# Performance work log

Hardware: AMD Instinct MI355X
Metric: run time of the kernel (lower is better)

## Reference

```python
import jax, jax.numpy as jnp
import numpy as np

N_NODES = 50000


def gcn_layer(x, W, b, src, dst, norm):
    # x: [N, Fin] -> [N, Fout]; PyG GCNConv: x' = D^-1/2 (A+I) D^-1/2 (x W) + b
    h = x @ W
    msg = h[src] * norm[:, None]              # gather + scale per edge (incl. self loops)
    out = jax.ops.segment_sum(msg, dst, num_segments=N_NODES)
    return out + b


def setup_inputs() -> dict:
    key = jax.random.key(0)
    ks = jax.random.split(key, 12)
    F_in, F_hid, T, E = 128, 128, 10, 1600000
    features = jax.random.normal(ks[0], (N_NODES, F_in), dtype=jnp.float32)
    edges = jax.random.randint(ks[1], (2, E), 0, N_NODES, dtype=jnp.int64)
    s = 1.0 / np.sqrt(F_in)
    W0 = jax.random.uniform(ks[2], (F_in, F_hid), jnp.float32, -s, s)
    b0 = jnp.zeros((F_hid,), jnp.float32)
    W1 = jax.random.uniform(ks[3], (F_hid, F_hid), jnp.float32, -s, s)
    b1 = jnp.zeros((F_hid,), jnp.float32)
    W2 = jax.random.uniform(ks[4], (F_hid, F_hid), jnp.float32, -s, s)
    b2 = jnp.zeros((F_hid,), jnp.float32)
    Wout = jax.random.uniform(ks[5], (F_hid, T), jnp.float32, -s, s)
    bout = jax.random.uniform(ks[6], (T,), jnp.float32, -s, s)
    return {"features": features, "edges": edges, "W0": W0, "b0": b0,
            "W1": W1, "b1": b1, "W2": W2, "b2": b2, "Wout": Wout, "bout": bout}


def reference(features, edges, W0, b0, W1, b1, W2, b2, Wout, bout):
    # Add self loops once; edge structure shared across layers.
    loop = jnp.arange(N_NODES, dtype=edges.dtype)
    src = jnp.concatenate([edges[0], loop])
    dst = jnp.concatenate([edges[1], loop])
    deg = jax.ops.segment_sum(jnp.ones_like(dst, dtype=features.dtype), dst,
                              num_segments=N_NODES)
    dinv = jnp.where(deg > 0, jax.lax.rsqrt(deg), 0.0)
    norm = dinv[src] * dinv[dst]              # [E + N]

    x = gcn_layer(features, W0, b0, src, dst, norm)
    x = gcn_layer(x, W1, b1, src, dst, norm)
    x = gcn_layer(x, W2, b2, src, dst, norm)

    pooled = jnp.mean(x, axis=0)              # [F_hid]
    logits = pooled @ Wout + bout             # [T]
    return jax.nn.log_softmax(logits, axis=0).reshape(1, -1)
```

## Files before the change

### kernel.cpp

```cpp
#include <hip/hip_runtime.h>


#define FDIM 128
#define HSZ 12500
#define NBG 64
#define NB_V0 512
#define S_FIX 16777216.0f
#define INV_S (1.0f / 16777216.0f)


__global__ void __launch_bounds__(1024)
hist_deg_kernel(const int* __restrict__ edges, int E, int e4, int N,
                int* __restrict__ partial) {
  __shared__ int h[HSZ];
  const int g = blockIdx.x / NBG;
  const int j = blockIdx.x - g * NBG;
  const int lo = g * HSZ;
  const int hi = min(N, lo + HSZ);
  const int hs = hi - lo;
  for (int i = threadIdx.x; i < hs; i += blockDim.x) h[i] = 0;
  __syncthreads();
  const int* dst = edges + E;
  const int4* dst4 = (const int4*)dst;
  for (int i = j * blockDim.x + threadIdx.x; i < e4; i += NBG * blockDim.x) {
    int4 d = dst4[i];
    if (d.x >= lo && d.x < hi) atomicAdd(&h[d.x - lo], 1);
    if (d.y >= lo && d.y < hi) atomicAdd(&h[d.y - lo], 1);
    if (d.z >= lo && d.z < hi) atomicAdd(&h[d.z - lo], 1);
    if (d.w >= lo && d.w < hi) atomicAdd(&h[d.w - lo], 1);
  }
  if (j == 0) {
    for (int e = 4 * e4 + threadIdx.x; e < E; e += blockDim.x) {
      int d = dst[e];
      if (d >= lo && d < hi) atomicAdd(&h[d - lo], 1);
    }
  }
  __syncthreads();
  int* out = partial + (size_t)blockIdx.x * HSZ;
  for (int i = threadIdx.x; i < hs; i += blockDim.x) out[i] = h[i];
}

__global__ void merge_dinv_kernel(const int* __restrict__ partial,
                                  float* __restrict__ dinv, int N) {
  int n = blockIdx.x * blockDim.x + threadIdx.x;
  if (n >= N) return;
  int g = n / HSZ;
  int off = n - g * HSZ;
  const int* p = partial + ((size_t)g * NBG) * HSZ + off;
  int s = 1;
  for (int jj = 0; jj < NBG; ++jj) s += p[(size_t)jj * HSZ];
  dinv[n] = rsqrtf((float)s);
}

__global__ void __launch_bounds__(1024)
hist_u_kernel(const int* __restrict__ edges, int E, int e4, int N,
              const float* __restrict__ w,
              float* __restrict__ partial) {
  __shared__ float h[HSZ];
  const int g = blockIdx.x / NBG;
  const int j = blockIdx.x - g * NBG;
  const int lo = g * HSZ;
  const int hi = min(N, lo + HSZ);
  const int hs = hi - lo;
  for (int i = threadIdx.x; i < hs; i += blockDim.x) h[i] = 0.f;
  __syncthreads();
  const int4* s4 = (const int4*)edges;
  const int4* d4 = (const int4*)(edges + E);
  for (int i = j * blockDim.x + threadIdx.x; i < e4; i += NBG * blockDim.x) {
    int4 s = s4[i];
    int4 d = d4[i];
    if (s.x >= lo && s.x < hi) atomicAdd(&h[s.x - lo], w[d.x]);
    if (s.y >= lo && s.y < hi) atomicAdd(&h[s.y - lo], w[d.y]);
    if (s.z >= lo && s.z < hi) atomicAdd(&h[s.z - lo], w[d.z]);
    if (s.w >= lo && s.w < hi) atomicAdd(&h[s.w - lo], w[d.w]);
  }
  if (j == 0) {
    const int* se = edges; const int* de = edges + E;
    for (int e = 4 * e4 + threadIdx.x; e < E; e += blockDim.x) {
      int s = se[e], d = de[e];
      if (s >= lo && s < hi) atomicAdd(&h[s - lo], w[d]);
    }
  }
  __syncthreads();
  float* out = partial + (size_t)blockIdx.x * HSZ;
  for (int i = threadIdx.x; i < hs; i += blockDim.x) out[i] = h[i];
}

__global__ void __launch_bounds__(256)
merge_u_kernel(const float* __restrict__ partial,
               const float* __restrict__ dinv,
               const float* __restrict__ win,
               float* __restrict__ uout,
               float* __restrict__ wout,
               float* __restrict__ ssump, int N) {
  __shared__ float red[4];
  int n = blockIdx.x * blockDim.x + threadIdx.x;
  float u = 0.f;
  if (n < N) {
    int g = n / HSZ;
    int off = n - g * HSZ;
    const float* p = partial + ((size_t)g * NBG) * HSZ + off;
    float s = 0.f;
    for (int jj = 0; jj < NBG; ++jj) s += p[(size_t)jj * HSZ];
    u = dinv[n] * (s + win[n]);
    if (uout) uout[n] = u;
    if (wout) wout[n] = dinv[n] * u;
  }
  if (ssump) {
    float a = u;
    for (int o = 32; o > 0; o >>= 1) a += __shfl_down(a, o, 64);
    if ((threadIdx.x & 63) == 0) red[threadIdx.x >> 6] = a;
    __syncthreads();
    if (threadIdx.x == 0)
      ssump[blockIdx.x] = red[0] + red[1] + red[2] + red[3];
  }
}

__global__ void v0_kernel(const float* __restrict__ feat,
                          const float* __restrict__ u0,
                          float* __restrict__ v0p, int N) {
  __shared__ float sh[2][FDIM];
  int f = threadIdx.x & (FDIM - 1);
  int r2 = threadIdx.x >> 7;
  float acc = 0.f;
  for (int r = blockIdx.x * 2 + r2; r < N; r += gridDim.x * 2)
    acc += u0[r] * feat[(size_t)r * FDIM + f];
  sh[r2][f] = acc;
  __syncthreads();
  if (r2 == 0) v0p[(size_t)blockIdx.x * FDIM + f] = sh[0][f] + sh[1][f];
}

__global__ void __launch_bounds__(1024)
final_kernel(const float* __restrict__ W0, const float* __restrict__ b0,
             const float* __restrict__ W1, const float* __restrict__ b1,
             const float* __restrict__ W2, const float* __restrict__ b2,
             const float* __restrict__ Wout, const float* __restrict__ bout,
             const float* __restrict__ v0p, int nv0,
             const float* __restrict__ ssumpA,
             const float* __restrict__ ssumpB,
             int nss,
             float* __restrict__ out, int N) {
  __shared__ float Wl[FDIM * FDIM];
  __shared__ float WoL[FDIM * 10];
  __shared__ float va[FDIM], vb[FDIM];
  __shared__ float part[8][FDIM];
  __shared__ float red0[16], red1[16];
  __shared__ float shS1, shS2;
  __shared__ float lg[10];
  const int t = threadIdx.x;
  const int f = t & (FDIM - 1);
  const int sl = t >> 7;

  {
    const float4* w4 = (const float4*)W0;
    float4* l4 = (float4*)Wl;
    #pragma unroll
    for (int i = 0; i < 4; ++i) l4[t + i * 1024] = w4[t + i * 1024];
    if (t < (FDIM * 10) / 4) ((float4*)WoL)[t] = ((const float4*)Wout)[t];
  }
  float acc = 0.f;
  for (int j = sl; j < nv0; j += 8) acc += v0p[(size_t)j * FDIM + f];
  part[sl][f] = acc;
  {
    float a0 = 0.f, a1 = 0.f;
    for (int j = t; j < nss; j += 1024) { a0 += ssumpA[j]; a1 += ssumpB[j]; }
    for (int o = 32; o > 0; o >>= 1) {
      a0 += __shfl_down(a0, o, 64);
      a1 += __shfl_down(a1, o, 64);
    }
    if ((t & 63) == 0) { red0[t >> 6] = a0; red1[t >> 6] = a1; }
  }
  __syncthreads();
  if (sl == 0) {
    float s = 0.f;
    #pragma unroll
    for (int j = 0; j < 8; ++j) s += part[j][f];
    va[f] = s;
  }
  if (t == 0) {
    float x = 0.f, y = 0.f;
    #pragma unroll
    for (int i = 0; i < 16; ++i) { x += red0[i]; y += red1[i]; }
    shS2 = x; shS1 = y;
  }
  __syncthreads();

  acc = 0.f;
  #pragma unroll
  for (int k = 0; k < 16; ++k) {
    int kk = sl * 16 + k;
    acc += va[kk] * Wl[kk * FDIM + f];
  }
  part[sl][f] = acc;
  __syncthreads();
  {
    const float4* w4 = (const float4*)W1;
    float4* l4 = (float4*)Wl;
    #pragma unroll
    for (int i = 0; i < 4; ++i) l4[t + i * 1024] = w4[t + i * 1024];
  }
  if (sl == 0) {
    float s = 0.f;
    #pragma unroll
    for (int j = 0; j < 8; ++j) s += part[j][f];
    vb[f] = s + shS1 * b0[f];
  }
  __syncthreads();

  acc = 0.f;
  #pragma unroll
  for (int k = 0; k < 16; ++k) {
    int kk = sl * 16 + k;
    acc += vb[kk] * Wl[kk * FDIM + f];
  }
  part[sl][f] = acc;
  __syncthreads();
  {
    const float4* w4 = (const float4*)W2;
    float4* l4 = (float4*)Wl;
    #pragma unroll
    for (int i = 0; i < 4; ++i) l4[t + i * 1024] = w4[t + i * 1024];
  }
  if (sl == 0) {
    float s = 0.f;
    #pragma unroll
    for (int j = 0; j < 8; ++j) s += part[j][f];
    va[f] = s + shS2 * b1[f];
  }
  __syncthreads();

  acc = 0.f;
  #pragma unroll
  for (int k = 0; k < 16; ++k) {
    int kk = sl * 16 + k;
    acc += va[kk] * Wl[kk * FDIM + f];
  }
  part[sl][f] = acc;
  __syncthreads();
  if (sl == 0) {
    float s = 0.f;
    #pragma unroll
    for (int j = 0; j < 8; ++j) s += part[j][f];
    vb[f] = s / (float)N + b2[f];
  }
  __syncthreads();

  if (t < 10) {
    float a = 0.f;
    for (int k = 0; k < FDIM; ++k) a += vb[k] * WoL[k * 10 + t];
    lg[t] = a + bout[t];
  }
  __syncthreads();
  if (t == 0) {
    float m = lg[0];
    for (int q = 1; q < 10; ++q) m = fmaxf(m, lg[q]);
    float s = 0.f;
    for (int q = 0; q < 10; ++q) s += expf(lg[q] - m);
    float lse = logf(s);
    for (int q = 0; q < 10; ++q) out[q] = lg[q] - m - lse;
  }
}


__global__ void deg_kernel(const int* __restrict__ edges, int E, int M,
                           int* __restrict__ deg) {
  for (int e = blockIdx.x * blockDim.x + threadIdx.x; e < M;
       e += gridDim.x * blockDim.x) {
    int d = (e < E) ? edges[E + e] : (e - E);
    atomicAdd(&deg[d], 1);
  }
}

__global__ void dinv_kernel(const int* __restrict__ deg,
                            float* __restrict__ dinv, int N) {
  int i = blockIdx.x * blockDim.x + threadIdx.x;
  if (i < N) {
    float d = (float)deg[i];
    dinv[i] = (d > 0.f) ? rsqrtf(d) : 0.f;
  }
}

__global__ void upass_kernel(const int* __restrict__ edges, int E, int M,
                             const float* __restrict__ dinv,
                             const int* __restrict__ uin_q,
                             int* __restrict__ uout_q) {
  for (int e = blockIdx.x * blockDim.x + threadIdx.x; e < M;
       e += gridDim.x * blockDim.x) {
    int s, d;
    if (e < E) { s = edges[e]; d = edges[E + e]; }
    else       { s = e - E;    d = s; }
    float v = dinv[s] * dinv[d];
    if (uin_q) v *= (float)uin_q[d] * INV_S;
    atomicAdd(&uout_q[s], __float2int_rn(v * S_FIX));
  }
}

__global__ void sums_kernel(const int* __restrict__ u2q,
                            const int* __restrict__ u1q,
                            float* __restrict__ ssump, int N) {
  __shared__ float red[8];
  int i = blockIdx.x * blockDim.x + threadIdx.x;
  float a = 0.f, b = 0.f;
  if (i < N) { a = (float)u2q[i] * INV_S; b = (float)u1q[i] * INV_S; }
  for (int o = 32; o > 0; o >>= 1) {
    a += __shfl_down(a, o, 64);
    b += __shfl_down(b, o, 64);
  }
  if ((threadIdx.x & 63) == 0) {
    red[(threadIdx.x >> 6) * 2] = a;
    red[(threadIdx.x >> 6) * 2 + 1] = b;
  }
  __syncthreads();
  if (threadIdx.x == 0) {
    ssump[blockIdx.x] = red[0] + red[2] + red[4] + red[6];
    ssump[gridDim.x + blockIdx.x] = red[1] + red[3] + red[5] + red[7];
  }
}

__global__ void v0_fallback_kernel(const float* __restrict__ feat,
                                   const int* __restrict__ u0q,
                                   float* __restrict__ v0p, int N) {
  __shared__ float sh[2][FDIM];
  int f = threadIdx.x & (FDIM - 1);
  int r2 = threadIdx.x >> 7;
  float acc = 0.f;
  for (int r = blockIdx.x * 2 + r2; r < N; r += gridDim.x * 2)
    acc += ((float)u0q[r] * INV_S) * feat[(size_t)r * FDIM + f];
  sh[r2][f] = acc;
  __syncthreads();
  if (r2 == 0) v0p[(size_t)blockIdx.x * FDIM + f] = sh[0][f] + sh[1][f];
}


extern "C" void kernel_launch(void* const* d_in, const int* in_sizes, int n_in,
                              void* d_out, int out_size, void* d_ws, size_t ws_size,
                              hipStream_t stream) {
  const float* feat = (const float*)d_in[0];
  const int*   edges = (const int*)d_in[1];
  const float* W0 = (const float*)d_in[2];
  const float* b0 = (const float*)d_in[3];
  const float* W1 = (const float*)d_in[4];
  const float* b1 = (const float*)d_in[5];
  const float* W2 = (const float*)d_in[6];
  const float* b2 = (const float*)d_in[7];
  const float* Wout = (const float*)d_in[8];
  const float* bout = (const float*)d_in[9];

  const int N = in_sizes[0] / FDIM;
  const int E = in_sizes[1] / 2;
  const int NG = (N + HSZ - 1) / HSZ;
  const int e4 = ((E & 3) == 0) ? (E >> 2) : 0;
  const int mergeGrid = (N + 255) / 256;

  char* ws = (char*)d_ws;
  size_t nb = ((size_t)N * 4 + 511) & ~(size_t)511;
  size_t partB = ((size_t)NG * NBG * HSZ * 4 + 511) & ~(size_t)511;
  size_t v0pB = (size_t)NB_V0 * FDIM * 4;
  size_t ssB = ((size_t)mergeGrid * 4 + 511) & ~(size_t)511;
  size_t need = partB + 4 * nb + v0pB + 2 * ssB;

  if (ws_size >= need) {
    char* p = ws;
    void*  part = (void*)p;        p += partB;
    float* dinv = (float*)p;       p += nb;
    float* w2   = (float*)p;       p += nb;
    float* w1   = (float*)p;       p += nb;
    float* u0   = (float*)p;       p += nb;
    float* v0p  = (float*)p;       p += v0pB;
    float* ssA  = (float*)p;       p += ssB;
    float* ssB_ = (float*)p;

    hist_deg_kernel<<<NG * NBG, 1024, 0, stream>>>(edges, E, e4, N, (int*)part);
    merge_dinv_kernel<<<mergeGrid, 256, 0, stream>>>((const int*)part, dinv, N);
    hist_u_kernel<<<NG * NBG, 1024, 0, stream>>>(edges, E, e4, N, dinv, (float*)part);
    merge_u_kernel<<<mergeGrid, 256, 0, stream>>>((const float*)part, dinv, dinv,
                                                  nullptr, w2, ssA, N);
    hist_u_kernel<<<NG * NBG, 1024, 0, stream>>>(edges, E, e4, N, w2, (float*)part);
    merge_u_kernel<<<mergeGrid, 256, 0, stream>>>((const float*)part, dinv, w2,
                                                  nullptr, w1, ssB_, N);
    hist_u_kernel<<<NG * NBG, 1024, 0, stream>>>(edges, E, e4, N, w1, (float*)part);
    merge_u_kernel<<<mergeGrid, 256, 0, stream>>>((const float*)part, dinv, w1,
                                                  u0, nullptr, nullptr, N);
    v0_kernel<<<NB_V0, 256, 0, stream>>>(feat, u0, v0p, N);
    final_kernel<<<1, 1024, 0, stream>>>(W0, b0, W1, b1, W2, b2, Wout, bout,
                                         v0p, NB_V0, ssA, ssB_, mergeGrid,
                                         (float*)d_out, N);
  } else {
    const int M = E + N;
    int*   deg  = (int*)(ws);
    float* dinv = (float*)(ws + nb);
    int*   u2q  = (int*)(ws + 2 * nb);
    int*   u1q  = (int*)(ws + 3 * nb);
    int*   u0q  = (int*)(ws + 4 * nb);
    float* v0p  = (float*)(ws + 5 * nb);
    float* ssp  = (float*)(ws + 5 * nb + v0pB);

    hipMemsetAsync(ws, 0, 5 * nb, stream);

    deg_kernel<<<2048, 256, 0, stream>>>(edges, E, M, deg);
    dinv_kernel<<<mergeGrid, 256, 0, stream>>>(deg, dinv, N);
    upass_kernel<<<2048, 256, 0, stream>>>(edges, E, M, dinv, nullptr, u2q);
    upass_kernel<<<2048, 256, 0, stream>>>(edges, E, M, dinv, u2q, u1q);
    upass_kernel<<<2048, 256, 0, stream>>>(edges, E, M, dinv, u1q, u0q);
    sums_kernel<<<mergeGrid, 256, 0, stream>>>(u2q, u1q, ssp, N);
    v0_fallback_kernel<<<NB_V0, 256, 0, stream>>>(feat, u0q, v0p, N);
    final_kernel<<<1, 1024, 0, stream>>>(W0, b0, W1, b1, W2, b2, Wout, bout,
                                         v0p, NB_V0, ssp, ssp + mergeGrid,
                                         mergeGrid, (float*)d_out, N);
  }
}
```

Before: 125.3 us.

## Bucket edges by source range once so histogram passes read only their slice

Adds count, scan and scatter kernels that sort edges into four buckets by source-node range, each edge packed as a local source index and a destination in one int. The three weighted-histogram passes then read only their group's bucket instead of rescanning all edges with range filters, which cuts their global traffic about eightfold. The v0 reduction is also reshaped to fewer blocks with more threads each. The packing assumes destinations fit in 16 bits (N=50000) and exactly four groups, which is only guarded by NG==4, and the one-time scatter costs three extra launches plus a full pass over the edges.

```diff
diff --git a/kernel.cpp b/kernel.cpp
--- a/kernel.cpp
+++ b/kernel.cpp
@@ -4,9 +4,124 @@
 #define FDIM 128
 #define HSZ 12500
 #define NBG 64
-#define NB_V0 512
+#define NB_V0 128
 #define S_FIX 16777216.0f
 #define INV_S (1.0f / 16777216.0f)
+
+
+__global__ void __launch_bounds__(256)
+count_kernel(const int* __restrict__ edges, int E, int e4,
+             int* __restrict__ blockCnt) {
+  __shared__ int cnt[4];
+  if (threadIdx.x < 4) cnt[threadIdx.x] = 0;
+  __syncthreads();
+  int c0 = 0, c1 = 0, c2 = 0, c3 = 0;
+  const int4* s4 = (const int4*)edges;
+  for (int i = blockIdx.x * 256 + threadIdx.x; i < e4; i += 256 * 256) {
+    int4 s = s4[i];
+    int g;
+    g = s.x / HSZ; if (g == 0) ++c0; else if (g == 1) ++c1; else if (g == 2) ++c2; else ++c3;
+    g = s.y / HSZ; if (g == 0) ++c0; else if (g == 1) ++c1; else if (g == 2) ++c2; else ++c3;
+    g = s.z / HSZ; if (g == 0) ++c0; else if (g == 1) ++c1; else if (g == 2) ++c2; else ++c3;
+    g = s.w / HSZ; if (g == 0) ++c0; else if (g == 1) ++c1; else if (g == 2) ++c2; else ++c3;
+  }
+  if (blockIdx.x == 0) {
+    for (int e = 4 * e4 + threadIdx.x; e < E; e += 256) {
+      int g = edges[e] / HSZ;
+      if (g == 0) ++c0; else if (g == 1) ++c1; else if (g == 2) ++c2; else ++c3;
+    }
+  }
+  for (int o = 32; o > 0; o >>= 1) {
+    c0 += __shfl_down(c0, o, 64);
+    c1 += __shfl_down(c1, o, 64);
+    c2 += __shfl_down(c2, o, 64);
+    c3 += __shfl_down(c3, o, 64);
+  }
+  if ((threadIdx.x & 63) == 0) {
+    atomicAdd(&cnt[0], c0);
+    atomicAdd(&cnt[1], c1);
+    atomicAdd(&cnt[2], c2);
+    atomicAdd(&cnt[3], c3);
+  }
+  __syncthreads();
+  if (threadIdx.x < 4) blockCnt[blockIdx.x * 4 + threadIdx.x] = cnt[threadIdx.x];
+}
+
+__global__ void __launch_bounds__(256)
+scan_kernel(const int* __restrict__ blockCnt, int* __restrict__ blockOff,
+            int* __restrict__ meta) {
+  __shared__ int c[256 * 4];
+  __shared__ int totS[4], baseS[4];
+  for (int i = threadIdx.x; i < 256 * 4; i += 256) c[i] = blockCnt[i];
+  __syncthreads();
+  if (threadIdx.x < 4) {
+    int g = threadIdx.x, run = 0;
+    for (int b = 0; b < 256; ++b) {
+      int v = c[b * 4 + g];
+      c[b * 4 + g] = run;
+      run += v;
+    }
+    totS[g] = run;
+  }
+  __syncthreads();
+  if (threadIdx.x == 0) {
+    int b = 0;
+    for (int g = 0; g < 4; ++g) { baseS[g] = b; b += totS[g]; }
+  }
+  __syncthreads();
+  for (int i = threadIdx.x; i < 256 * 4; i += 256)
+    blockOff[i] = c[i] + baseS[i & 3];
+  if (threadIdx.x < 4) {
+    meta[threadIdx.x] = baseS[threadIdx.x];
+    meta[4 + threadIdx.x] = totS[threadIdx.x];
+  }
+}
+
+__device__ __forceinline__ void push_edge(int s, int d, int lane, int w,
+                                          int* off, volatile int* wbase,
+                                          int* __restrict__ bucket) {
+  int g = s / HSZ;
+  unsigned long long m0 = __ballot(g == 0);
+  unsigned long long m1 = __ballot(g == 1);
+  unsigned long long m2 = __ballot(g == 2);
+  unsigned long long m3 = __ballot(g == 3);
+  unsigned long long mg = (g == 0) ? m0 : (g == 1) ? m1 : (g == 2) ? m2 : m3;
+  #pragma unroll
+  for (int k = 0; k < 4; ++k) {
+    unsigned long long mk = (k == 0) ? m0 : (k == 1) ? m1 : (k == 2) ? m2 : m3;
+    int ck = __popcll(mk);
+    if (ck && lane == __ffsll((unsigned long long)mk) - 1)
+      wbase[w * 4 + k] = atomicAdd(&off[k], ck);
+  }
+  int rank = __popcll(mg & ((1ull << lane) - 1ull));
+  bucket[wbase[w * 4 + g] + rank] = ((s - g * HSZ) << 16) | d;
+}
+
+__global__ void __launch_bounds__(256)
+scatter_kernel(const int* __restrict__ edges, int E, int e4,
+               const int* __restrict__ blockOff, int* __restrict__ bucket) {
+  __shared__ int off[4];
+  __shared__ int wbase[4 * 4];
+  if (threadIdx.x < 4) off[threadIdx.x] = blockOff[blockIdx.x * 4 + threadIdx.x];
+  __syncthreads();
+  const int lane = threadIdx.x & 63;
+  const int w = threadIdx.x >> 6;
+  const int4* s4 = (const int4*)edges;
+  const int4* d4 = (const int4*)(edges + E);
+  for (int i = blockIdx.x * 256 + threadIdx.x; i < e4; i += 256 * 256) {
+    int4 s = s4[i];
+    int4 d = d4[i];
+    push_edge(s.x, d.x, lane, w, off, wbase, bucket);
+    push_edge(s.y, d.y, lane, w, off, wbase, bucket);
+    push_edge(s.z, d.z, lane, w, off, wbase, bucket);
+    push_edge(s.w, d.w, lane, w, off, wbase, bucket);
+  }
+  if (blockIdx.x == 0) {
+    for (int e = 4 * e4 + threadIdx.x; e < E; e += 256) {
+      push_edge(edges[e], edges[E + e], lane, w, off, wbase, bucket);
+    }
+  }
+}
 
 
 __global__ void __launch_bounds__(1024)
@@ -53,37 +168,25 @@
 }
 
 __global__ void __launch_bounds__(1024)
-hist_u_kernel(const int* __restrict__ edges, int E, int e4, int N,
-              const float* __restrict__ w,
+hist_u_kernel(const int* __restrict__ bucket, const int* __restrict__ meta,
+              int N, const float* __restrict__ w,
               float* __restrict__ partial) {
   __shared__ float h[HSZ];
   const int g = blockIdx.x / NBG;
   const int j = blockIdx.x - g * NBG;
   const int lo = g * HSZ;
-  const int hi = min(N, lo + HSZ);
-  const int hs = hi - lo;
-  for (int i = threadIdx.x; i < hs; i += blockDim.x) h[i] = 0.f;
-  __syncthreads();
-  const int4* s4 = (const int4*)edges;
-  const int4* d4 = (const int4*)(edges + E);
-  for (int i = j * blockDim.x + threadIdx.x; i < e4; i += NBG * blockDim.x) {
-    int4 s = s4[i];
-    int4 d = d4[i];
-    if (s.x >= lo && s.x < hi) atomicAdd(&h[s.x - lo], w[d.x]);
-    if (s.y >= lo && s.y < hi) atomicAdd(&h[s.y - lo], w[d.y]);
-    if (s.z >= lo && s.z < hi) atomicAdd(&h[s.z - lo], w[d.z]);
-    if (s.w >= lo && s.w < hi) atomicAdd(&h[s.w - lo], w[d.w]);
-  }
-  if (j == 0) {
-    const int* se = edges; const int* de = edges + E;
-    for (int e = 4 * e4 + threadIdx.x; e < E; e += blockDim.x) {
-      int s = se[e], d = de[e];
-      if (s >= lo && s < hi) atomicAdd(&h[s - lo], w[d]);
-    }
+  const int hs = min(N, lo + HSZ) - lo;
+  for (int i = threadIdx.x; i < hs; i += 1024) h[i] = 0.f;
+  __syncthreads();
+  const int base = meta[g];
+  const int end = base + meta[4 + g];
+  for (int i = base + j * 1024 + threadIdx.x; i < end; i += NBG * 1024) {
+    int p = bucket[i];
+    atomicAdd(&h[p >> 16], w[p & 0xFFFF]);
   }
   __syncthreads();
   float* out = partial + (size_t)blockIdx.x * HSZ;
-  for (int i = threadIdx.x; i < hs; i += blockDim.x) out[i] = h[i];
+  for (int i = threadIdx.x; i < hs; i += 1024) out[i] = h[i];
 }
 
 __global__ void __launch_bounds__(256)
@@ -116,18 +219,23 @@
   }
 }
 
-__global__ void v0_kernel(const float* __restrict__ feat,
-                          const float* __restrict__ u0,
-                          float* __restrict__ v0p, int N) {
-  __shared__ float sh[2][FDIM];
+__global__ void __launch_bounds__(1024)
+v0_kernel(const float* __restrict__ feat, const float* __restrict__ u0,
+          float* __restrict__ v0p, int N) {
+  __shared__ float sh[8][FDIM];
   int f = threadIdx.x & (FDIM - 1);
-  int r2 = threadIdx.x >> 7;
+  int r8 = threadIdx.x >> 7;
   float acc = 0.f;
-  for (int r = blockIdx.x * 2 + r2; r < N; r += gridDim.x * 2)
+  for (int r = blockIdx.x * 8 + r8; r < N; r += NB_V0 * 8)
     acc += u0[r] * feat[(size_t)r * FDIM + f];
-  sh[r2][f] = acc;
-  __syncthreads();
-  if (r2 == 0) v0p[(size_t)blockIdx.x * FDIM + f] = sh[0][f] + sh[1][f];
+  sh[r8][f] = acc;
+  __syncthreads();
+  if (r8 == 0) {
+    float s = acc;
+    #pragma unroll
+    for (int k = 1; k < 8; ++k) s += sh[k][f];
+    v0p[(size_t)blockIdx.x * FDIM + f] = s;
+  }
 }
 
 __global__ void __launch_bounds__(1024)
@@ -349,17 +457,18 @@
   const int N = in_sizes[0] / FDIM;
   const int E = in_sizes[1] / 2;
   const int NG = (N + HSZ - 1) / HSZ;
-  const int e4 = ((E & 3) == 0) ? (E >> 2) : 0;
+  const int e4 = E >> 2;
   const int mergeGrid = (N + 255) / 256;
 
   char* ws = (char*)d_ws;
   size_t nb = ((size_t)N * 4 + 511) & ~(size_t)511;
   size_t partB = ((size_t)NG * NBG * HSZ * 4 + 511) & ~(size_t)511;
-  size_t v0pB = (size_t)NB_V0 * FDIM * 4;
+  size_t v0pB = ((size_t)NB_V0 * FDIM * 4 + 511) & ~(size_t)511;
   size_t ssB = ((size_t)mergeGrid * 4 + 511) & ~(size_t)511;
-  size_t need = partB + 4 * nb + v0pB + 2 * ssB;
-
-  if (ws_size >= need) {
+  size_t bktB = ((size_t)E * 4 + 511) & ~(size_t)511;
+  size_t need = partB + 4 * nb + v0pB + 2 * ssB + bktB + 16384;
+
+  if (ws_size >= need && NG == 4) {
     char* p = ws;
     void*  part = (void*)p;        p += partB;
     float* dinv = (float*)p;       p += nb;
@@ -368,20 +477,27 @@
     float* u0   = (float*)p;       p += nb;
     float* v0p  = (float*)p;       p += v0pB;
     float* ssA  = (float*)p;       p += ssB;
-    float* ssB_ = (float*)p;
-
+    float* ssB_ = (float*)p;       p += ssB;
+    int*   bucket = (int*)p;       p += bktB;
+    int*   blockCnt = (int*)p;     p += 4096;
+    int*   blockOff = (int*)p;     p += 4096;
+    int*   meta = (int*)p;
+
+    count_kernel<<<256, 256, 0, stream>>>(edges, E, e4, blockCnt);
+    scan_kernel<<<1, 256, 0, stream>>>(blockCnt, blockOff, meta);
+    scatter_kernel<<<256, 256, 0, stream>>>(edges, E, e4, blockOff, bucket);
     hist_deg_kernel<<<NG * NBG, 1024, 0, stream>>>(edges, E, e4, N, (int*)part);
     merge_dinv_kernel<<<mergeGrid, 256, 0, stream>>>((const int*)part, dinv, N);
-    hist_u_kernel<<<NG * NBG, 1024, 0, stream>>>(edges, E, e4, N, dinv, (float*)part);
+    hist_u_kernel<<<NG * NBG, 1024, 0, stream>>>(bucket, meta, N, dinv, (float*)part);
     merge_u_kernel<<<mergeGrid, 256, 0, stream>>>((const float*)part, dinv, dinv,
                                                   nullptr, w2, ssA, N);
-    hist_u_kernel<<<NG * NBG, 1024, 0, stream>>>(edges, E, e4, N, w2, (float*)part);
+    hist_u_kernel<<<NG * NBG, 1024, 0, stream>>>(bucket, meta, N, w2, (float*)part);
     merge_u_kernel<<<mergeGrid, 256, 0, stream>>>((const float*)part, dinv, w2,
                                                   nullptr, w1, ssB_, N);
-    hist_u_kernel<<<NG * NBG, 1024, 0, stream>>>(edges, E, e4, N, w1, (float*)part);
+    hist_u_kernel<<<NG * NBG, 1024, 0, stream>>>(bucket, meta, N, w1, (float*)part);
     merge_u_kernel<<<mergeGrid, 256, 0, stream>>>((const float*)part, dinv, w1,
                                                   u0, nullptr, nullptr, N);
-    v0_kernel<<<NB_V0, 256, 0, stream>>>(feat, u0, v0p, N);
+    v0_kernel<<<NB_V0, 1024, 0, stream>>>(feat, u0, v0p, N);
     final_kernel<<<1, 1024, 0, stream>>>(W0, b0, W1, b1, W2, b2, Wout, bout,
                                          v0p, NB_V0, ssA, ssB_, mergeGrid,
                                          (float*)d_out, N);
```

Result: slower. 141.8 us (+13.1%).

## Fuse all histogram, merge and reduction stages into one cooperative kernel

Applied to the files above, without the earlier changes.

Replaces the chain of about ten kernel launches with a single cooperative mega-kernel of 256 blocks by 1024 threads. It uses grid.sync between the degree histogram, the three weight-propagation passes, the feature reduction and the final dense tail. The goal is to remove per-launch overhead and inter-kernel gaps. The old atomic fallback path is dropped and the function now returns early unless N fits in exactly four histogram groups, which hardcodes the problem shape. It also relies on the cooperative launch succeeding with one block per CU.

```diff
diff --git a/kernel.cpp b/kernel.cpp
--- a/kernel.cpp
+++ b/kernel.cpp
@@ -1,12 +1,252 @@
 #include <hip/hip_runtime.h>
+#include <hip/hip_cooperative_groups.h>
+
+namespace cg = cooperative_groups;
 
 
 #define FDIM 128
 #define HSZ 12500
 #define NBG 64
-#define NB_V0 512
+#define NBLK 256
+#define NTHR 1024
 #define S_FIX 16777216.0f
 #define INV_S (1.0f / 16777216.0f)
+
+
+__global__ void __launch_bounds__(1024, 1)
+mega_kernel(const float* __restrict__ feat, const int* __restrict__ edges,
+            const float* __restrict__ W0, const float* __restrict__ b0,
+            const float* __restrict__ W1, const float* __restrict__ b1,
+            const float* __restrict__ W2, const float* __restrict__ b2,
+            const float* __restrict__ Wout, const float* __restrict__ bout,
+            int E, int e4, int N,
+            float* __restrict__ part, float* __restrict__ dinv,
+            float* __restrict__ w2, float* __restrict__ w1,
+            float* __restrict__ u0, float* __restrict__ v0p,
+            float* __restrict__ ssA, float* __restrict__ ssB,
+            float* __restrict__ out) {
+  cg::grid_group grid = cg::this_grid();
+  __shared__ float h[HSZ];
+  __shared__ float va[FDIM], vb[FDIM];
+  __shared__ float partS[8][FDIM];
+  __shared__ float red0[16], red1[16];
+  __shared__ float lg[10];
+  __shared__ float shS1, shS2;
+
+  const int t = threadIdx.x;
+  const int bid = blockIdx.x;
+  const int g = bid >> 6;
+  const int j = bid & (NBG - 1);
+  const int lo = g * HSZ;
+  const int hs = min(N, lo + HSZ) - lo;
+  const int4* s4 = (const int4*)edges;
+  const int4* d4 = (const int4*)(edges + E);
+
+  {
+    int* hi_ = (int*)h;
+    for (int i = t; i < hs; i += NTHR) hi_[i] = 0;
+    __syncthreads();
+    for (int i = j * NTHR + t; i < e4; i += NBG * NTHR) {
+      int4 d = d4[i];
+      if (d.x >= lo && d.x < lo + hs) atomicAdd(&hi_[d.x - lo], 1);
+      if (d.y >= lo && d.y < lo + hs) atomicAdd(&hi_[d.y - lo], 1);
+      if (d.z >= lo && d.z < lo + hs) atomicAdd(&hi_[d.z - lo], 1);
+      if (d.w >= lo && d.w < lo + hs) atomicAdd(&hi_[d.w - lo], 1);
+    }
+    if (j == 0) {
+      const int* dst = edges + E;
+      for (int e = 4 * e4 + t; e < E; e += NTHR) {
+        int d = dst[e];
+        if (d >= lo && d < lo + hs) atomicAdd(&hi_[d - lo], 1);
+      }
+    }
+    __syncthreads();
+    int* op = (int*)part + (size_t)bid * HSZ;
+    for (int i = t; i < hs; i += NTHR) op[i] = hi_[i];
+  }
+  grid.sync();
+
+  {
+    int n = bid * NTHR + t;
+    if (n < N) {
+      int gg = n / HSZ, off = n - gg * HSZ;
+      const int* p = (const int*)part + ((size_t)gg * NBG) * HSZ + off;
+      int s = 1;
+      for (int jj = 0; jj < NBG; ++jj) s += p[(size_t)jj * HSZ];
+      dinv[n] = rsqrtf((float)s);
+    }
+  }
+  grid.sync();
+
+  #pragma unroll 1
+  for (int pass = 0; pass < 3; ++pass) {
+    const float* w = (pass == 0) ? dinv : (pass == 1) ? w2 : w1;
+    for (int i = t; i < hs; i += NTHR) h[i] = 0.f;
+    __syncthreads();
+    for (int i = j * NTHR + t; i < e4; i += NBG * NTHR) {
+      int4 s = s4[i];
+      int4 d = d4[i];
+      if (s.x >= lo && s.x < lo + hs) atomicAdd(&h[s.x - lo], w[d.x]);
+      if (s.y >= lo && s.y < lo + hs) atomicAdd(&h[s.y - lo], w[d.y]);
+      if (s.z >= lo && s.z < lo + hs) atomicAdd(&h[s.z - lo], w[d.z]);
+      if (s.w >= lo && s.w < lo + hs) atomicAdd(&h[s.w - lo], w[d.w]);
+    }
+    if (j == 0) {
+      for (int e = 4 * e4 + t; e < E; e += NTHR) {
+        int s = edges[e], d = edges[E + e];
+        if (s >= lo && s < lo + hs) atomicAdd(&h[s - lo], w[d]);
+      }
+    }
+    __syncthreads();
+    {
+      float* op = part + (size_t)bid * HSZ;
+      for (int i = t; i < hs; i += NTHR) op[i] = h[i];
+    }
+    grid.sync();
+
+    {
+      int n = bid * NTHR + t;
+      float u = 0.f;
+      if (n < N) {
+        int gg = n / HSZ, off = n - gg * HSZ;
+        const float* p = part + ((size_t)gg * NBG) * HSZ + off;
+        float s = 0.f;
+        for (int jj = 0; jj < NBG; ++jj) s += p[(size_t)jj * HSZ];
+        u = dinv[n] * (s + w[n]);
+        if (pass == 0)      w2[n] = dinv[n] * u;
+        else if (pass == 1) w1[n] = dinv[n] * u;
+        else                u0[n] = u;
+      }
+      if (pass < 2) {
+        float a = u;
+        for (int o = 32; o > 0; o >>= 1) a += __shfl_down(a, o, 64);
+        if ((t & 63) == 0) red0[t >> 6] = a;
+        __syncthreads();
+        if (t == 0) {
+          float s = 0.f;
+          #pragma unroll
+          for (int i = 0; i < 16; ++i) s += red0[i];
+          if (pass == 0) ssA[bid] = s; else ssB[bid] = s;
+        }
+        __syncthreads();
+      }
+    }
+    grid.sync();
+  }
+
+  {
+    int f = t & (FDIM - 1);
+    int r8 = t >> 7;
+    float acc = 0.f;
+    for (int r = bid * 8 + r8; r < N; r += NBLK * 8)
+      acc += u0[r] * feat[(size_t)r * FDIM + f];
+    partS[r8][f] = acc;
+    __syncthreads();
+    if (r8 == 0) {
+      float s = acc;
+      #pragma unroll
+      for (int k = 1; k < 8; ++k) s += partS[k][f];
+      v0p[(size_t)bid * FDIM + f] = s;
+    }
+  }
+  grid.sync();
+
+  if (bid != 0) return;
+  {
+    const int f = t & (FDIM - 1);
+    const int sl = t >> 7;
+    if (t < (FDIM * 10) / 4) ((float4*)h)[t] = ((const float4*)Wout)[t];
+    float acc = 0.f;
+    for (int jj = sl; jj < NBLK; jj += 8) acc += v0p[(size_t)jj * FDIM + f];
+    partS[sl][f] = acc;
+    {
+      float a0 = (t < NBLK) ? ssA[t] : 0.f;
+      float a1 = (t < NBLK) ? ssB[t] : 0.f;
+      for (int o = 32; o > 0; o >>= 1) {
+        a0 += __shfl_down(a0, o, 64);
+        a1 += __shfl_down(a1, o, 64);
+      }
+      if ((t & 63) == 0) { red0[t >> 6] = a0; red1[t >> 6] = a1; }
+    }
+    __syncthreads();
+    if (sl == 0) {
+      float s = 0.f;
+      #pragma unroll
+      for (int jj = 0; jj < 8; ++jj) s += partS[jj][f];
+      va[f] = s;
+    }
+    if (t == 0) {
+      float x = 0.f, y = 0.f;
+      #pragma unroll
+      for (int i = 0; i < 16; ++i) { x += red0[i]; y += red1[i]; }
+      shS2 = x; shS1 = y;
+    }
+    __syncthreads();
+
+    acc = 0.f;
+    #pragma unroll
+    for (int k = 0; k < 16; ++k) {
+      int kk = sl * 16 + k;
+      acc += va[kk] * W0[kk * FDIM + f];
+    }
+    partS[sl][f] = acc;
+    __syncthreads();
+    if (sl == 0) {
+      float s = 0.f;
+      #pragma unroll
+      for (int jj = 0; jj < 8; ++jj) s += partS[jj][f];
+      vb[f] = s + shS1 * b0[f];
+    }
+    __syncthreads();
+
+    acc = 0.f;
+    #pragma unroll
+    for (int k = 0; k < 16; ++k) {
+      int kk = sl * 16 + k;
+      acc += vb[kk] * W1[kk * FDIM + f];
+    }
+    partS[sl][f] = acc;
+    __syncthreads();
+    if (sl == 0) {
+      float s = 0.f;
+      #pragma unroll
+      for (int jj = 0; jj < 8; ++jj) s += partS[jj][f];
+      va[f] = s + shS2 * b1[f];
+    }
+    __syncthreads();
+
+    acc = 0.f;
+    #pragma unroll
+    for (int k = 0; k < 16; ++k) {
+      int kk = sl * 16 + k;
+      acc += va[kk] * W2[kk * FDIM + f];
+    }
+    partS[sl][f] = acc;
+    __syncthreads();
+    if (sl == 0) {
+      float s = 0.f;
+      #pragma unroll
+      for (int jj = 0; jj < 8; ++jj) s += partS[jj][f];
+      vb[f] = s / (float)N + b2[f];
+    }
+    __syncthreads();
+
+    if (t < 10) {
+      float a = 0.f;
+      for (int k = 0; k < FDIM; ++k) a += vb[k] * h[k * 10 + t];
+      lg[t] = a + bout[t];
+    }
+    __syncthreads();
+    if (t == 0) {
+      float m = lg[0];
+      for (int q = 1; q < 10; ++q) m = fmaxf(m, lg[q]);
+      float s = 0.f;
+      for (int q = 0; q < 10; ++q) s += expf(lg[q] - m);
+      float lse = logf(s);
+      for (int q = 0; q < 10; ++q) out[q] = lg[q] - m - lse;
+    }
+  }
+}
 
 
 __global__ void __launch_bounds__(1024)
@@ -116,18 +356,23 @@
   }
 }
 
-__global__ void v0_kernel(const float* __restrict__ feat,
-                          const float* __restrict__ u0,
-                          float* __restrict__ v0p, int N) {
-  __shared__ float sh[2][FDIM];
+__global__ void __launch_bounds__(1024)
+v0_kernel(const float* __restrict__ feat, const float* __restrict__ u0,
+          float* __restrict__ v0p, int N) {
+  __shared__ float sh[8][FDIM];
   int f = threadIdx.x & (FDIM - 1);
-  int r2 = threadIdx.x >> 7;
+  int r8 = threadIdx.x >> 7;
   float acc = 0.f;
-  for (int r = blockIdx.x * 2 + r2; r < N; r += gridDim.x * 2)
+  for (int r = blockIdx.x * 8 + r8; r < N; r += 128 * 8)
     acc += u0[r] * feat[(size_t)r * FDIM + f];
-  sh[r2][f] = acc;
-  __syncthreads();
-  if (r2 == 0) v0p[(size_t)blockIdx.x * FDIM + f] = sh[0][f] + sh[1][f];
+  sh[r8][f] = acc;
+  __syncthreads();
+  if (r8 == 0) {
+    float s = acc;
+    #pragma unroll
+    for (int k = 1; k < 8; ++k) s += sh[k][f];
+    v0p[(size_t)blockIdx.x * FDIM + f] = s;
+  }
 }
 
 __global__ void __launch_bounds__(1024)
@@ -262,76 +507,6 @@
 }
 
 
-__global__ void deg_kernel(const int* __restrict__ edges, int E, int M,
-                           int* __restrict__ deg) {
-  for (int e = blockIdx.x * blockDim.x + threadIdx.x; e < M;
-       e += gridDim.x * blockDim.x) {
-    int d = (e < E) ? edges[E + e] : (e - E);
-    atomicAdd(&deg[d], 1);
-  }
-}
-
-__global__ void dinv_kernel(const int* __restrict__ deg,
-                            float* __restrict__ dinv, int N) {
-  int i = blockIdx.x * blockDim.x + threadIdx.x;
-  if (i < N) {
-    float d = (float)deg[i];
-    dinv[i] = (d > 0.f) ? rsqrtf(d) : 0.f;
-  }
-}
-
-__global__ void upass_kernel(const int* __restrict__ edges, int E, int M,
-                             const float* __restrict__ dinv,
-                             const int* __restrict__ uin_q,
-                             int* __restrict__ uout_q) {
-  for (int e = blockIdx.x * blockDim.x + threadIdx.x; e < M;
-       e += gridDim.x * blockDim.x) {
-    int s, d;
-    if (e < E) { s = edges[e]; d = edges[E + e]; }
-    else       { s = e - E;    d = s; }
-    float v = dinv[s] * dinv[d];
-    if (uin_q) v *= (float)uin_q[d] * INV_S;
-    atomicAdd(&uout_q[s], __float2int_rn(v * S_FIX));
-  }
-}
-
-__global__ void sums_kernel(const int* __restrict__ u2q,
-                            const int* __restrict__ u1q,
-                            float* __restrict__ ssump, int N) {
-  __shared__ float red[8];
-  int i = blockIdx.x * blockDim.x + threadIdx.x;
-  float a = 0.f, b = 0.f;
-  if (i < N) { a = (float)u2q[i] * INV_S; b = (float)u1q[i] * INV_S; }
-  for (int o = 32; o > 0; o >>= 1) {
-    a += __shfl_down(a, o, 64);
-    b += __shfl_down(b, o, 64);
-  }
-  if ((threadIdx.x & 63) == 0) {
-    red[(threadIdx.x >> 6) * 2] = a;
-    red[(threadIdx.x >> 6) * 2 + 1] = b;
-  }
-  __syncthreads();
-  if (threadIdx.x == 0) {
-    ssump[blockIdx.x] = red[0] + red[2] + red[4] + red[6];
-    ssump[gridDim.x + blockIdx.x] = red[1] + red[3] + red[5] + red[7];
-  }
-}
-
-__global__ void v0_fallback_kernel(const float* __restrict__ feat,
-                                   const int* __restrict__ u0q,
-                                   float* __restrict__ v0p, int N) {
-  __shared__ float sh[2][FDIM];
-  int f = threadIdx.x & (FDIM - 1);
-  int r2 = threadIdx.x >> 7;
-  float acc = 0.f;
-  for (int r = blockIdx.x * 2 + r2; r < N; r += gridDim.x * 2)
-    acc += ((float)u0q[r] * INV_S) * feat[(size_t)r * FDIM + f];
-  sh[r2][f] = acc;
-  __syncthreads();
-  if (r2 == 0) v0p[(size_t)blockIdx.x * FDIM + f] = sh[0][f] + sh[1][f];
-}
-
-
 extern "C" void kernel_launch(void* const* d_in, const int* in_sizes, int n_in,
                               void* d_out, int out_size, void* d_ws, size_t ws_size,
                               hipStream_t stream) {
@@ -349,63 +524,58 @@
   const int N = in_sizes[0] / FDIM;
   const int E = in_sizes[1] / 2;
   const int NG = (N + HSZ - 1) / HSZ;
-  const int e4 = ((E & 3) == 0) ? (E >> 2) : 0;
+  const int e4 = E >> 2;
   const int mergeGrid = (N + 255) / 256;
 
   char* ws = (char*)d_ws;
   size_t nb = ((size_t)N * 4 + 511) & ~(size_t)511;
-  size_t partB = ((size_t)NG * NBG * HSZ * 4 + 511) & ~(size_t)511;
-  size_t v0pB = (size_t)NB_V0 * FDIM * 4;
-  size_t ssB = ((size_t)mergeGrid * 4 + 511) & ~(size_t)511;
-  size_t need = partB + 4 * nb + v0pB + 2 * ssB;
-
-  if (ws_size >= need) {
-    char* p = ws;
-    void*  part = (void*)p;        p += partB;
-    float* dinv = (float*)p;       p += nb;
-    float* w2   = (float*)p;       p += nb;
-    float* w1   = (float*)p;       p += nb;
-    float* u0   = (float*)p;       p += nb;
-    float* v0p  = (float*)p;       p += v0pB;
-    float* ssA  = (float*)p;       p += ssB;
-    float* ssB_ = (float*)p;
-
-    hist_deg_kernel<<<NG * NBG, 1024, 0, stream>>>(edges, E, e4, N, (int*)part);
-    merge_dinv_kernel<<<mergeGrid, 256, 0, stream>>>((const int*)part, dinv, N);
-    hist_u_kernel<<<NG * NBG, 1024, 0, stream>>>(edges, E, e4, N, dinv, (float*)part);
-    merge_u_kernel<<<mergeGrid, 256, 0, stream>>>((const float*)part, dinv, dinv,
-                                                  nullptr, w2, ssA, N);
-    hist_u_kernel<<<NG * NBG, 1024, 0, stream>>>(edges, E, e4, N, w2, (float*)part);
-    merge_u_kernel<<<mergeGrid, 256, 0, stream>>>((const float*)part, dinv, w2,
-                                                  nullptr, w1, ssB_, N);
-    hist_u_kernel<<<NG * NBG, 1024, 0, stream>>>(edges, E, e4, N, w1, (float*)part);
-    merge_u_kernel<<<mergeGrid, 256, 0, stream>>>((const float*)part, dinv, w1,
-                                                  u0, nullptr, nullptr, N);
-    v0_kernel<<<NB_V0, 256, 0, stream>>>(feat, u0, v0p, N);
-    final_kernel<<<1, 1024, 0, stream>>>(W0, b0, W1, b1, W2, b2, Wout, bout,
-                                         v0p, NB_V0, ssA, ssB_, mergeGrid,
-                                         (float*)d_out, N);
-  } else {
-    const int M = E + N;
-    int*   deg  = (int*)(ws);
-    float* dinv = (float*)(ws + nb);
-    int*   u2q  = (int*)(ws + 2 * nb);
-    int*   u1q  = (int*)(ws + 3 * nb);
-    int*   u0q  = (int*)(ws + 4 * nb);
-    float* v0p  = (float*)(ws + 5 * nb);
-    float* ssp  = (float*)(ws + 5 * nb + v0pB);
-
-    hipMemsetAsync(ws, 0, 5 * nb, stream);
-
-    deg_kernel<<<2048, 256, 0, stream>>>(edges, E, M, deg);
-    dinv_kernel<<<mergeGrid, 256, 0, stream>>>(deg, dinv, N);
-    upass_kernel<<<2048, 256, 0, stream>>>(edges, E, M, dinv, nullptr, u2q);
-    upass_kernel<<<2048, 256, 0, stream>>>(edges, E, M, dinv, u2q, u1q);
-    upass_kernel<<<2048, 256, 0, stream>>>(edges, E, M, dinv, u1q, u0q);
-    sums_kernel<<<mergeGrid, 256, 0, stream>>>(u2q, u1q, ssp, N);
-    v0_fallback_kernel<<<NB_V0, 256, 0, stream>>>(feat, u0q, v0p, N);
-    final_kernel<<<1, 1024, 0, stream>>>(W0, b0, W1, b1, W2, b2, Wout, bout,
-                                         v0p, NB_V0, ssp, ssp + mergeGrid,
-                                         mergeGrid, (float*)d_out, N);
-  }
-}
+  size_t partB = ((size_t)4 * NBG * HSZ * 4 + 511) & ~(size_t)511;
+  size_t v0pB = ((size_t)NBLK * FDIM * 4 + 511) & ~(size_t)511;
+  size_t ssBsz = ((size_t)NBLK * 4 + 511) & ~(size_t)511;
+  size_t need = partB + 4 * nb + v0pB + 2 * ssBsz;
+
+  if (ws_size < need || NG != 4 || N > 4 * HSZ) {
+    return;
+  }
+
+  char* p = ws;
+  float* part = (float*)p;       p += partB;
+  float* dinv = (float*)p;       p += nb;
+  float* w2   = (float*)p;       p += nb;
+  float* w1   = (float*)p;       p += nb;
+  float* u0   = (float*)p;       p += nb;
+  float* v0p  = (float*)p;       p += v0pB;
+  float* ssA  = (float*)p;       p += ssBsz;
+  float* ssB_ = (float*)p;
+
+  {
+    void* args[] = {
+      (void*)&feat, (void*)&edges,
+      (void*)&W0, (void*)&b0, (void*)&W1, (void*)&b1,
+      (void*)&W2, (void*)&b2, (void*)&Wout, (void*)&bout,
+      (void*)&E, (void*)&e4, (void*)&N,
+      (void*)&part, (void*)&dinv, (void*)&w2, (void*)&w1,
+      (void*)&u0, (void*)&v0p, (void*)&ssA, (void*)&ssB_,
+      (void*)&d_out,
+    };
+    hipError_t err = hipLaunchCooperativeKernel(
+        (const void*)mega_kernel, dim3(NBLK), dim3(NTHR), args, 0, stream);
+    if (err == hipSuccess) return;
+  }
+
+  hist_deg_kernel<<<4 * NBG, 1024, 0, stream>>>(edges, E, e4, N, (int*)part);
+  merge_dinv_kernel<<<mergeGrid, 256, 0, stream>>>((const int*)part, dinv, N);
+  hist_u_kernel<<<4 * NBG, 1024, 0, stream>>>(edges, E, e4, N, dinv, part);
+  merge_u_kernel<<<mergeGrid, 256, 0, stream>>>(part, dinv, dinv,
+                                                nullptr, w2, ssA, N);
+  hist_u_kernel<<<4 * NBG, 1024, 0, stream>>>(edges, E, e4, N, w2, part);
+  merge_u_kernel<<<mergeGrid, 256, 0, stream>>>(part, dinv, w2,
+                                                nullptr, w1, ssB_, N);
+  hist_u_kernel<<<4 * NBG, 1024, 0, stream>>>(edges, E, e4, N, w1, part);
+  merge_u_kernel<<<mergeGrid, 256, 0, stream>>>(part, dinv, w1,
+                                                u0, nullptr, nullptr, N);
+  v0_kernel<<<128, 1024, 0, stream>>>(feat, u0, v0p, N);
+  final_kernel<<<1, 1024, 0, stream>>>(W0, b0, W1, b1, W2, b2, Wout, bout,
+                                       v0p, 128, ssA, ssB_, mergeGrid,
+                                       (float*)d_out, N);
+}
```

Result: slower. 388.3 us (+209.9%).
